# Optimization experiments

Hardware: AMD Instinct MI355X
Metric: run time of the kernel (lower is better)

## Reference

```python
import jax, jax.numpy as jnp
import numpy as np

N = 100000      # nodes
E = 1250000     # edges
D_IN = 64
D_OUT = 64


def _gconv(x, src, dst, W_rel, W_root, b, n_nodes):
    # PyG GraphConv (aggr='add'): out = lin_rel(sum_{j in N(i)} x_j) + lin_root(x_i)
    agg = jax.ops.segment_sum(x[src], dst, num_segments=n_nodes)  # [N, d]
    return agg @ W_rel + b + x @ W_root


def setup_inputs() -> dict:
    key = jax.random.key(0)
    ks = jax.random.split(key, 12)
    graph = jax.random.normal(ks[0], (N, D_IN), dtype=jnp.float32)
    edge_index = jax.random.randint(ks[1], (2, E), 0, N, dtype=jnp.int32)
    s_in = 1.0 / np.sqrt(D_IN)
    s_out = 1.0 / np.sqrt(D_OUT)
    d = {
        "graph": graph,
        "edge_index": edge_index,
        "W1_rel": jax.random.uniform(ks[2], (D_IN, D_OUT), jnp.float32, -s_in, s_in),
        "W1_root": jax.random.uniform(ks[3], (D_IN, D_OUT), jnp.float32, -s_in, s_in),
        "b1": jnp.zeros((D_OUT,), jnp.float32),
        "W2_rel": jax.random.uniform(ks[4], (D_OUT, D_OUT), jnp.float32, -s_out, s_out),
        "W2_root": jax.random.uniform(ks[5], (D_OUT, D_OUT), jnp.float32, -s_out, s_out),
        "b2": jnp.zeros((D_OUT,), jnp.float32),
        "W3_rel": jax.random.uniform(ks[6], (D_OUT, D_OUT), jnp.float32, -s_out, s_out),
        "W3_root": jax.random.uniform(ks[7], (D_OUT, D_OUT), jnp.float32, -s_out, s_out),
        "b3": jnp.zeros((D_OUT,), jnp.float32),
    }
    return d


def reference(graph, edge_index, W1_rel, W1_root, b1, W2_rel, W2_root, b2, W3_rel, W3_root, b3):
    src, dst = edge_index[0], edge_index[1]
    n = graph.shape[0]
    y1 = jax.nn.elu(_gconv(graph, src, dst, W1_rel, W1_root, b1, n))
    y2 = jax.nn.elu(_gconv(y1, src, dst, W2_rel, W2_root, b2, n))
    y3 = jax.nn.sigmoid(_gconv(y2, src, dst, W3_rel, W3_root, b3, n))
    return (y1, y2, y3)
```

## Files before the change

kernel.cpp:

```cpp
#include <hip/hip_runtime.h>
#include <hip/hip_bf16.h>
#include <math.h>


#define D 64
#define BSHIFT 9
#define BW 512
#define BCAP 8192

typedef __attribute__((ext_vector_type(8))) short short8;
typedef __attribute__((ext_vector_type(4))) float f32x4;

__device__ __forceinline__ ushort f2b(float f) {
    uint x = __float_as_uint(f);
    uint r = (x + 0x7fffu + ((x >> 16) & 1u)) >> 16;
    return (ushort)r;
}


__global__ __launch_bounds__(256) void convert_w(const float* __restrict__ w0,
                                                 const float* __restrict__ w1,
                                                 const float* __restrict__ w2,
                                                 const float* __restrict__ w3,
                                                 const float* __restrict__ w4,
                                                 const float* __restrict__ w5,
                                                 ushort* __restrict__ out,
                                                 int* __restrict__ bucketCnt,
                                                 ushort* __restrict__ hrel_zrow) {
    if (blockIdx.x == 0 && threadIdx.x < 256) bucketCnt[threadIdx.x] = 0;
    if (blockIdx.x == 1 && threadIdx.x < 32) ((uint*)hrel_zrow)[threadIdx.x] = 0;
    int m = blockIdx.x >> 4;
    int t = (blockIdx.x & 15) * 256 + threadIdx.x;
    const float* src = m == 0 ? w0 : m == 1 ? w1 : m == 2 ? w2 : m == 3 ? w3 : m == 4 ? w4 : w5;
    int k = t >> 6, d = t & 63;
    out[m * 4096 + d * 64 + k] = f2b(src[t]);
}


__global__ __launch_bounds__(1024) void bucket_scatter(const int* __restrict__ src,
                                                       const int* __restrict__ dst,
                                                       int* __restrict__ bucketCnt,
                                                       uint* __restrict__ store,
                                                       int E) {
    __shared__ int h[256], base[256], cur[256];
    int t = threadIdx.x;
    if (t < 256) { h[t] = 0; cur[t] = 0; }
    __syncthreads();
    int e = blockIdx.x * 1024 + t;
    uint rec = 0; int b = 0;
    bool ok = e < E;
    if (ok) {
        int s = src[e];
        int d = dst[e];
        b = d >> BSHIFT;
        rec = ((uint)(d & (BW - 1)) << 17) | (uint)s;
        atomicAdd(&h[b], 1);
    }
    __syncthreads();
    if (t < 256) base[t] = h[t] ? atomicAdd(&bucketCnt[t], h[t]) : 0;
    __syncthreads();
    if (ok) {
        int r = atomicAdd(&cur[b], 1);
        int pos = base[b] + r;
        if (pos < BCAP)
            store[(size_t)b * BCAP + pos] = rec;
    }
}


__global__ __launch_bounds__(256) void scan_buckets(const int* __restrict__ bucketCnt,
                                                    int* __restrict__ bucketBase,
                                                    int* __restrict__ offs,
                                                    int nb, int n, int E) {
    __shared__ int tmp[256];
    int t = threadIdx.x;
    int v = (t < nb) ? bucketCnt[t] : 0;
    tmp[t] = v;
    __syncthreads();
    for (int off = 1; off < 256; off <<= 1) {
        int add = (t >= off) ? tmp[t - off] : 0;
        __syncthreads();
        tmp[t] += add;
        __syncthreads();
    }
    if (t < nb) bucketBase[t] = tmp[t] - v;
    if (t == 0) offs[n] = E;
}


__global__ __launch_bounds__(1024) void bucket_build(const int* __restrict__ bucketCnt,
                                                     const int* __restrict__ bucketBase,
                                                     const uint* __restrict__ store,
                                                     int* __restrict__ offs,
                                                     int* __restrict__ src_sorted, int n) {
    __shared__ int h[BW], loc[BW], cur[BW];
    __shared__ uint se[BCAP];
    int b = blockIdx.x, t = threadIdx.x;
    int cnt = bucketCnt[b];
    if (cnt > BCAP) cnt = BCAP;
    int obase = bucketBase[b];
    int d0 = b << BSHIFT;
    int nd = n - d0;
    if (nd > BW) nd = BW;
    if (t < BW) { h[t] = 0; cur[t] = 0; }
    __syncthreads();
    for (int i = t; i < cnt; i += 1024) {
        uint p = store[(size_t)b * BCAP + i];
        se[i] = p;
        atomicAdd(&h[p >> 17], 1);
    }
    __syncthreads();
    if (t < BW) loc[t] = h[t];
    __syncthreads();
    for (int off = 1; off < BW; off <<= 1) {
        int add = (t < BW && t >= off) ? loc[t - off] : 0;
        __syncthreads();
        if (t < BW) loc[t] += add;
        __syncthreads();
    }
    if (t < nd) offs[d0 + t] = obase + loc[t] - h[t];
    __syncthreads();
    for (int i = t; i < cnt; i += 1024) {
        uint p = se[i];
        int dl = p >> 17;
        int r = atomicAdd(&cur[dl], 1);
        src_sorted[obase + loc[dl] - h[dl] + r] = (int)(p & 0x1FFFFu);
    }
}


__global__ __launch_bounds__(256) void gemm_ro(const float* __restrict__ x,
                                               const ushort* __restrict__ WtR,
                                               const ushort* __restrict__ WtO,
                                               const float* __restrict__ bias,
                                               ushort* __restrict__ hrel,
                                               ushort* __restrict__ hroot, int n) {
    __shared__ ushort hsR[4][16 * 64];
    __shared__ ushort hsO[4][16 * 64];
    int t = threadIdx.x;
    int w = t >> 6, l = t & 63;
    int i0 = blockIdx.x * 64 + w * 16;
    int lr = l & 15, kb = l >> 4;
    int row = i0 + lr;
    int rowc = row < n ? row : n - 1;

    short8 a[2];
#pragma unroll
    for (int s = 0; s < 2; ++s) {
        const float* p = x + (size_t)rowc * D + s * 32 + kb * 8;
        float4 u = *(const float4*)p;
        float4 v = *(const float4*)(p + 4);
        a[s][0] = f2b(u.x); a[s][1] = f2b(u.y); a[s][2] = f2b(u.z); a[s][3] = f2b(u.w);
        a[s][4] = f2b(v.x); a[s][5] = f2b(v.y); a[s][6] = f2b(v.z); a[s][7] = f2b(v.w);
    }

#pragma unroll
    for (int ct = 0; ct < 4; ++ct) {
        f32x4 accR = (f32x4){0.f, 0.f, 0.f, 0.f};
        f32x4 accO = (f32x4){0.f, 0.f, 0.f, 0.f};
#pragma unroll
        for (int s = 0; s < 2; ++s) {
            short8 bR = *(const short8*)(WtR + (ct * 16 + lr) * D + s * 32 + kb * 8);
            short8 bO = *(const short8*)(WtO + (ct * 16 + lr) * D + s * 32 + kb * 8);
            accR = __builtin_amdgcn_mfma_f32_16x16x32_bf16(a[s], bR, accR, 0, 0, 0);
            accO = __builtin_amdgcn_mfma_f32_16x16x32_bf16(a[s], bO, accO, 0, 0, 0);
        }
        float bv = bias[ct * 16 + lr];
#pragma unroll
        for (int i = 0; i < 4; ++i) {
            hsR[w][(kb * 4 + i) * 64 + ct * 16 + lr] = f2b(accR[i]);
            hsO[w][(kb * 4 + i) * 64 + ct * 16 + lr] = f2b(accO[i] + bv);
        }
    }
    __syncthreads();

    int r = l >> 2, ch = l & 3;
    int grow = i0 + r;
    if (grow < n) {
        const float4* spR = (const float4*)&hsR[w][r * 64 + ch * 16];
        const float4* spO = (const float4*)&hsO[w][r * 64 + ch * 16];
        float4 r0 = spR[0];
        float4 r1 = spR[1];
        float4 o0 = spO[0];
        float4 o1 = spO[1];
        *(float4*)(hrel + (size_t)grow * D + ch * 16) = r0;
        *(float4*)(hrel + (size_t)grow * D + ch * 16 + 8) = r1;
        *(float4*)(hroot + (size_t)grow * D + ch * 16) = o0;
        *(float4*)(hroot + (size_t)grow * D + ch * 16 + 8) = o1;
    }
}


template <int ACT>
__global__ __launch_bounds__(256) void agg_act(const ushort* __restrict__ hrel,
                                               const ushort* __restrict__ hroot,
                                               const int* __restrict__ offs,
                                               const int* __restrict__ srcs,
                                               float* __restrict__ y, int n) {
    int nA = blockIdx.x * 8 + (threadIdx.x >> 6) * 2;
    int l = threadIdx.x & 63;
    if (nA >= n) return;
    int nB = nA + 1;
    bool hasB = nB < n;
    int q = l >> 4, r = l & 15;

    int oA = offs[nA];
    int oB = offs[nA + 1];
    int oC = hasB ? offs[nA + 2] : oB;

    float a0 = 0.f, a1 = 0.f, a2 = 0.f, a3 = 0.f;
    float b0 = 0.f, b1 = 0.f, b2 = 0.f, b3 = 0.f;

    int eA = oA, eB = oB;
    while (eA < oB || eB < oC) {
#pragma unroll
        for (int k = 0; k < 4; ++k) {
            int ia = eA + k * 4 + q;
            int ib = eB + k * 4 + q;
            int sA = (ia < oB) ? srcs[ia] : n;
            int sB = (ib < oC) ? srcs[ib] : n;
            uint2 uA = *(const uint2*)(hrel + (size_t)sA * D + r * 4);
            uint2 uB = *(const uint2*)(hrel + (size_t)sB * D + r * 4);
            a0 += __uint_as_float(uA.x << 16);
            a1 += __uint_as_float(uA.x & 0xffff0000u);
            a2 += __uint_as_float(uA.y << 16);
            a3 += __uint_as_float(uA.y & 0xffff0000u);
            b0 += __uint_as_float(uB.x << 16);
            b1 += __uint_as_float(uB.x & 0xffff0000u);
            b2 += __uint_as_float(uB.y << 16);
            b3 += __uint_as_float(uB.y & 0xffff0000u);
        }
        eA += 16; eB += 16;
    }

    a0 += __shfl_xor(a0, 32); a0 += __shfl_xor(a0, 16);
    a1 += __shfl_xor(a1, 32); a1 += __shfl_xor(a1, 16);
    a2 += __shfl_xor(a2, 32); a2 += __shfl_xor(a2, 16);
    a3 += __shfl_xor(a3, 32); a3 += __shfl_xor(a3, 16);
    b0 += __shfl_xor(b0, 32); b0 += __shfl_xor(b0, 16);
    b1 += __shfl_xor(b1, 32); b1 += __shfl_xor(b1, 16);
    b2 += __shfl_xor(b2, 32); b2 += __shfl_xor(b2, 16);
    b3 += __shfl_xor(b3, 32); b3 += __shfl_xor(b3, 16);

    if (q < 2 && (q == 0 || hasB)) {
        int node = q == 0 ? nA : nB;
        float v0 = q == 0 ? a0 : b0;
        float v1 = q == 0 ? a1 : b1;
        float v2 = q == 0 ? a2 : b2;
        float v3 = q == 0 ? a3 : b3;
        uint2 hr = *(const uint2*)(hroot + (size_t)node * D + r * 4);
        v0 += __uint_as_float(hr.x << 16);
        v1 += __uint_as_float(hr.x & 0xffff0000u);
        v2 += __uint_as_float(hr.y << 16);
        v3 += __uint_as_float(hr.y & 0xffff0000u);
        if (ACT == 0) {
            v0 = v0 > 0.f ? v0 : __expf(v0) - 1.f;
            v1 = v1 > 0.f ? v1 : __expf(v1) - 1.f;
            v2 = v2 > 0.f ? v2 : __expf(v2) - 1.f;
            v3 = v3 > 0.f ? v3 : __expf(v3) - 1.f;
        } else {
            v0 = __builtin_amdgcn_rcpf(1.f + __expf(-v0));
            v1 = __builtin_amdgcn_rcpf(1.f + __expf(-v1));
            v2 = __builtin_amdgcn_rcpf(1.f + __expf(-v2));
            v3 = __builtin_amdgcn_rcpf(1.f + __expf(-v3));
        }
        float4 o; o.x = v0; o.y = v1; o.z = v2; o.w = v3;
        *(float4*)(y + (size_t)node * D + r * 4) = o;
    }
}


extern "C" void kernel_launch(void* const* d_in, const int* in_sizes, int n_in,
                              void* d_out, int out_size, void* d_ws, size_t ws_size,
                              hipStream_t stream) {
    const float* graph = (const float*)d_in[0];
    const int* eidx    = (const int*)d_in[1];
    const float* W1r = (const float*)d_in[2];
    const float* W1o = (const float*)d_in[3];
    const float* b1  = (const float*)d_in[4];
    const float* W2r = (const float*)d_in[5];
    const float* W2o = (const float*)d_in[6];
    const float* b2  = (const float*)d_in[7];
    const float* W3r = (const float*)d_in[8];
    const float* W3o = (const float*)d_in[9];
    const float* b3  = (const float*)d_in[10];

    int n = in_sizes[0] / D;
    int E = in_sizes[1] / 2;
    const int* src  = eidx;
    const int* dstl = eidx + E;
    int nb = (n + BW - 1) >> BSHIFT;

    char* w = (char*)d_ws;
    auto carve = [&](size_t bytes) {
        void* p = (void*)w;
        w += (bytes + 255) & ~(size_t)255;
        return p;
    };
    ushort* hrel  = (ushort*)carve((size_t)(n + 1) * D * sizeof(ushort));
    ushort* hroot = (ushort*)carve((size_t)n * D * sizeof(ushort));
    uint* store = (uint*)hrel;
    int* offs       = (int*)carve((size_t)(n + 1) * sizeof(int));
    int* src_sorted = (int*)carve((size_t)(E + 16) * sizeof(int));
    int* bucketCnt  = (int*)carve(256 * sizeof(int));
    int* bucketBase = (int*)carve(256 * sizeof(int));
    ushort* wt      = (ushort*)carve(6 * 4096 * sizeof(ushort));
    ushort* wtR1 = wt;
    ushort* wtO1 = wt + 1 * 4096;
    ushort* wtR2 = wt + 2 * 4096;
    ushort* wtO2 = wt + 3 * 4096;
    ushort* wtR3 = wt + 4 * 4096;
    ushort* wtO3 = wt + 5 * 4096;

    int eb1 = (E + 1023) / 1024;
    int tb  = (n + 63) / 64;
    int ab  = (n + 7) / 8;

    convert_w<<<96, 256, 0, stream>>>(W1r, W1o, W2r, W2o, W3r, W3o, wt, bucketCnt,
                                      hrel + (size_t)n * D);
    bucket_scatter<<<eb1, 1024, 0, stream>>>(src, dstl, bucketCnt, store, E);
    scan_buckets<<<1, 256, 0, stream>>>(bucketCnt, bucketBase, offs, nb, n, E);
    bucket_build<<<nb, 1024, 0, stream>>>(bucketCnt, bucketBase, store, offs, src_sorted, n);

    float* out = (float*)d_out;
    float* y1 = out;
    float* y2 = out + (size_t)n * D;
    float* y3 = out + 2 * (size_t)n * D;


    gemm_ro<<<tb, 256, 0, stream>>>(graph, wtR1, wtO1, b1, hrel, hroot, n);
    agg_act<0><<<ab, 256, 0, stream>>>(hrel, hroot, offs, src_sorted, y1, n);
    gemm_ro<<<tb, 256, 0, stream>>>(y1, wtR2, wtO2, b2, hrel, hroot, n);
    agg_act<0><<<ab, 256, 0, stream>>>(hrel, hroot, offs, src_sorted, y2, n);
    gemm_ro<<<tb, 256, 0, stream>>>(y2, wtR3, wtO3, b3, hrel, hroot, n);
    agg_act<1><<<ab, 256, 0, stream>>>(hrel, hroot, offs, src_sorted, y3, n);
}
```

Measured before the change: 316.5 us.

## Fuse edge bucket scatter with first-layer GEMM and fold bucket scan into build

Merges the edge bucket-scatter kernel and the first layer's dense transform into one launch, with block ranges split by role, so the two independent phases run concurrently. The bucket prefix scan now runs inside each bucket_build block, which drops a separate single-block kernel. The scatter staging buffer moves from hrel to the y3 output region so the first GEMM can write hrel at the same time. It also hoists the root-term load in the aggregation kernel ahead of the neighbour loop. In exchange, every build block repeats a small 256-entry scan, and the scatter now uses 256-thread blocks that each handle four edges per thread.

```diff
diff --git a/kernel.cpp b/kernel.cpp
--- a/kernel.cpp
+++ b/kernel.cpp
@@ -37,109 +37,16 @@
 }
 
 
-__global__ __launch_bounds__(1024) void bucket_scatter(const int* __restrict__ src,
-                                                       const int* __restrict__ dst,
-                                                       int* __restrict__ bucketCnt,
-                                                       uint* __restrict__ store,
-                                                       int E) {
-    __shared__ int h[256], base[256], cur[256];
-    int t = threadIdx.x;
-    if (t < 256) { h[t] = 0; cur[t] = 0; }
-    __syncthreads();
-    int e = blockIdx.x * 1024 + t;
-    uint rec = 0; int b = 0;
-    bool ok = e < E;
-    if (ok) {
-        int s = src[e];
-        int d = dst[e];
-        b = d >> BSHIFT;
-        rec = ((uint)(d & (BW - 1)) << 17) | (uint)s;
-        atomicAdd(&h[b], 1);
-    }
-    __syncthreads();
-    if (t < 256) base[t] = h[t] ? atomicAdd(&bucketCnt[t], h[t]) : 0;
-    __syncthreads();
-    if (ok) {
-        int r = atomicAdd(&cur[b], 1);
-        int pos = base[b] + r;
-        if (pos < BCAP)
-            store[(size_t)b * BCAP + pos] = rec;
-    }
-}
-
-
-__global__ __launch_bounds__(256) void scan_buckets(const int* __restrict__ bucketCnt,
-                                                    int* __restrict__ bucketBase,
-                                                    int* __restrict__ offs,
-                                                    int nb, int n, int E) {
-    __shared__ int tmp[256];
-    int t = threadIdx.x;
-    int v = (t < nb) ? bucketCnt[t] : 0;
-    tmp[t] = v;
-    __syncthreads();
-    for (int off = 1; off < 256; off <<= 1) {
-        int add = (t >= off) ? tmp[t - off] : 0;
-        __syncthreads();
-        tmp[t] += add;
-        __syncthreads();
-    }
-    if (t < nb) bucketBase[t] = tmp[t] - v;
-    if (t == 0) offs[n] = E;
-}
-
-
-__global__ __launch_bounds__(1024) void bucket_build(const int* __restrict__ bucketCnt,
-                                                     const int* __restrict__ bucketBase,
-                                                     const uint* __restrict__ store,
-                                                     int* __restrict__ offs,
-                                                     int* __restrict__ src_sorted, int n) {
-    __shared__ int h[BW], loc[BW], cur[BW];
-    __shared__ uint se[BCAP];
-    int b = blockIdx.x, t = threadIdx.x;
-    int cnt = bucketCnt[b];
-    if (cnt > BCAP) cnt = BCAP;
-    int obase = bucketBase[b];
-    int d0 = b << BSHIFT;
-    int nd = n - d0;
-    if (nd > BW) nd = BW;
-    if (t < BW) { h[t] = 0; cur[t] = 0; }
-    __syncthreads();
-    for (int i = t; i < cnt; i += 1024) {
-        uint p = store[(size_t)b * BCAP + i];
-        se[i] = p;
-        atomicAdd(&h[p >> 17], 1);
-    }
-    __syncthreads();
-    if (t < BW) loc[t] = h[t];
-    __syncthreads();
-    for (int off = 1; off < BW; off <<= 1) {
-        int add = (t < BW && t >= off) ? loc[t - off] : 0;
-        __syncthreads();
-        if (t < BW) loc[t] += add;
-        __syncthreads();
-    }
-    if (t < nd) offs[d0 + t] = obase + loc[t] - h[t];
-    __syncthreads();
-    for (int i = t; i < cnt; i += 1024) {
-        uint p = se[i];
-        int dl = p >> 17;
-        int r = atomicAdd(&cur[dl], 1);
-        src_sorted[obase + loc[dl] - h[dl] + r] = (int)(p & 0x1FFFFu);
-    }
-}
-
-
-__global__ __launch_bounds__(256) void gemm_ro(const float* __restrict__ x,
-                                               const ushort* __restrict__ WtR,
-                                               const ushort* __restrict__ WtO,
-                                               const float* __restrict__ bias,
-                                               ushort* __restrict__ hrel,
-                                               ushort* __restrict__ hroot, int n) {
-    __shared__ ushort hsR[4][16 * 64];
-    __shared__ ushort hsO[4][16 * 64];
-    int t = threadIdx.x;
+__device__ __forceinline__ void gemm_ro_body(int blk, int t,
+                                             const float* __restrict__ x,
+                                             const ushort* __restrict__ WtR,
+                                             const ushort* __restrict__ WtO,
+                                             const float* __restrict__ bias,
+                                             ushort* __restrict__ hrel,
+                                             ushort* __restrict__ hroot, int n,
+                                             ushort* hsR, ushort* hsO) {
     int w = t >> 6, l = t & 63;
-    int i0 = blockIdx.x * 64 + w * 16;
+    int i0 = blk * 64 + w * 16;
     int lr = l & 15, kb = l >> 4;
     int row = i0 + lr;
     int rowc = row < n ? row : n - 1;
@@ -154,6 +61,8 @@
         a[s][4] = f2b(v.x); a[s][5] = f2b(v.y); a[s][6] = f2b(v.z); a[s][7] = f2b(v.w);
     }
 
+    ushort* hR = hsR + w * 16 * 64;
+    ushort* hO = hsO + w * 16 * 64;
 #pragma unroll
     for (int ct = 0; ct < 4; ++ct) {
         f32x4 accR = (f32x4){0.f, 0.f, 0.f, 0.f};
@@ -168,8 +77,8 @@
         float bv = bias[ct * 16 + lr];
 #pragma unroll
         for (int i = 0; i < 4; ++i) {
-            hsR[w][(kb * 4 + i) * 64 + ct * 16 + lr] = f2b(accR[i]);
-            hsO[w][(kb * 4 + i) * 64 + ct * 16 + lr] = f2b(accO[i] + bv);
+            hR[(kb * 4 + i) * 64 + ct * 16 + lr] = f2b(accR[i]);
+            hO[(kb * 4 + i) * 64 + ct * 16 + lr] = f2b(accO[i] + bv);
         }
     }
     __syncthreads();
@@ -177,8 +86,8 @@
     int r = l >> 2, ch = l & 3;
     int grow = i0 + r;
     if (grow < n) {
-        const float4* spR = (const float4*)&hsR[w][r * 64 + ch * 16];
-        const float4* spO = (const float4*)&hsO[w][r * 64 + ch * 16];
+        const float4* spR = (const float4*)&hR[r * 64 + ch * 16];
+        const float4* spO = (const float4*)&hO[r * 64 + ch * 16];
         float4 r0 = spR[0];
         float4 r1 = spR[1];
         float4 o0 = spO[0];
@@ -187,6 +96,121 @@
         *(float4*)(hrel + (size_t)grow * D + ch * 16 + 8) = r1;
         *(float4*)(hroot + (size_t)grow * D + ch * 16) = o0;
         *(float4*)(hroot + (size_t)grow * D + ch * 16 + 8) = o1;
+    }
+}
+
+__global__ __launch_bounds__(256) void gemm_ro(const float* __restrict__ x,
+                                               const ushort* __restrict__ WtR,
+                                               const ushort* __restrict__ WtO,
+                                               const float* __restrict__ bias,
+                                               ushort* __restrict__ hrel,
+                                               ushort* __restrict__ hroot, int n) {
+    __shared__ ushort hsR[4 * 16 * 64];
+    __shared__ ushort hsO[4 * 16 * 64];
+    gemm_ro_body(blockIdx.x, threadIdx.x, x, WtR, WtO, bias, hrel, hroot, n, hsR, hsO);
+}
+
+
+__global__ __launch_bounds__(256) void scatter_gemm(const int* __restrict__ esrc,
+                                                    const int* __restrict__ edst,
+                                                    int* __restrict__ bucketCnt,
+                                                    uint* __restrict__ store,
+                                                    int E, int SB,
+                                                    const float* __restrict__ x,
+                                                    const ushort* __restrict__ WtR,
+                                                    const ushort* __restrict__ WtO,
+                                                    const float* __restrict__ bias,
+                                                    ushort* __restrict__ hrel,
+                                                    ushort* __restrict__ hroot, int n) {
+    __shared__ ushort hsR[4 * 16 * 64];
+    int t = threadIdx.x;
+    int bx = blockIdx.x;
+    if (bx >= SB) {
+        __shared__ ushort hsO[4 * 16 * 64];
+        gemm_ro_body(bx - SB, t, x, WtR, WtO, bias, hrel, hroot, n, hsR, hsO);
+        return;
+    }
+    int* h    = (int*)hsR;
+    int* base = h + 256;
+    int* cur  = base + 256;
+    if (t < 256) { h[t] = 0; cur[t] = 0; }
+    __syncthreads();
+    int e0 = bx * 1024;
+    uint rec[4]; int bb[4];
+#pragma unroll
+    for (int i = 0; i < 4; ++i) {
+        int e = e0 + i * 256 + t;
+        if (e < E) {
+            int s = esrc[e];
+            int d = edst[e];
+            bb[i] = d >> BSHIFT;
+            rec[i] = ((uint)(d & (BW - 1)) << 17) | (uint)s;
+            atomicAdd(&h[bb[i]], 1);
+        } else bb[i] = -1;
+    }
+    __syncthreads();
+    base[t] = h[t] ? atomicAdd(&bucketCnt[t], h[t]) : 0;
+    __syncthreads();
+#pragma unroll
+    for (int i = 0; i < 4; ++i) {
+        if (bb[i] >= 0) {
+            int p = base[bb[i]] + atomicAdd(&cur[bb[i]], 1);
+            if (p < BCAP)
+                store[(size_t)bb[i] * BCAP + p] = rec[i];
+        }
+    }
+}
+
+
+__global__ __launch_bounds__(1024) void bucket_build(const int* __restrict__ bucketCnt,
+                                                     const uint* __restrict__ store,
+                                                     int* __restrict__ offs,
+                                                     int* __restrict__ src_sorted,
+                                                     int n, int nb, int E) {
+    __shared__ int h[BW], loc[BW], cur[BW];
+    __shared__ int sc[256];
+    __shared__ uint se[BCAP];
+    int b = blockIdx.x, t = threadIdx.x;
+
+    if (t < 256) sc[t] = (t < nb) ? bucketCnt[t] : 0;
+    __syncthreads();
+    for (int off = 1; off < 256; off <<= 1) {
+        int add = (t < 256 && t >= off) ? sc[t - off] : 0;
+        __syncthreads();
+        if (t < 256) sc[t] += add;
+        __syncthreads();
+    }
+    int obase = sc[b] - bucketCnt[b];
+    if (b == 0 && t == 0) offs[n] = E;
+
+    int cnt = bucketCnt[b];
+    if (cnt > BCAP) cnt = BCAP;
+    int d0 = b << BSHIFT;
+    int nd = n - d0;
+    if (nd > BW) nd = BW;
+    if (t < BW) { h[t] = 0; cur[t] = 0; }
+    __syncthreads();
+    for (int i = t; i < cnt; i += 1024) {
+        uint p = store[(size_t)b * BCAP + i];
+        se[i] = p;
+        atomicAdd(&h[p >> 17], 1);
+    }
+    __syncthreads();
+    if (t < BW) loc[t] = h[t];
+    __syncthreads();
+    for (int off = 1; off < BW; off <<= 1) {
+        int add = (t < BW && t >= off) ? loc[t - off] : 0;
+        __syncthreads();
+        if (t < BW) loc[t] += add;
+        __syncthreads();
+    }
+    if (t < nd) offs[d0 + t] = obase + loc[t] - h[t];
+    __syncthreads();
+    for (int i = t; i < cnt; i += 1024) {
+        uint p = se[i];
+        int dl = p >> 17;
+        int r = atomicAdd(&cur[dl], 1);
+        src_sorted[obase + loc[dl] - h[dl] + r] = (int)(p & 0x1FFFFu);
     }
 }
 
@@ -207,6 +231,9 @@
     int oA = offs[nA];
     int oB = offs[nA + 1];
     int oC = hasB ? offs[nA + 2] : oB;
+
+    uint2 hrA = *(const uint2*)(hroot + (size_t)nA * D + r * 4);
+    uint2 hrB = hasB ? *(const uint2*)(hroot + (size_t)nB * D + r * 4) : hrA;
 
     float a0 = 0.f, a1 = 0.f, a2 = 0.f, a3 = 0.f;
     float b0 = 0.f, b1 = 0.f, b2 = 0.f, b3 = 0.f;
@@ -244,15 +271,11 @@
 
     if (q < 2 && (q == 0 || hasB)) {
         int node = q == 0 ? nA : nB;
-        float v0 = q == 0 ? a0 : b0;
-        float v1 = q == 0 ? a1 : b1;
-        float v2 = q == 0 ? a2 : b2;
-        float v3 = q == 0 ? a3 : b3;
-        uint2 hr = *(const uint2*)(hroot + (size_t)node * D + r * 4);
-        v0 += __uint_as_float(hr.x << 16);
-        v1 += __uint_as_float(hr.x & 0xffff0000u);
-        v2 += __uint_as_float(hr.y << 16);
-        v3 += __uint_as_float(hr.y & 0xffff0000u);
+        uint2 hr = q == 0 ? hrA : hrB;
+        float v0 = (q == 0 ? a0 : b0) + __uint_as_float(hr.x << 16);
+        float v1 = (q == 0 ? a1 : b1) + __uint_as_float(hr.x & 0xffff0000u);
+        float v2 = (q == 0 ? a2 : b2) + __uint_as_float(hr.y << 16);
+        float v3 = (q == 0 ? a3 : b3) + __uint_as_float(hr.y & 0xffff0000u);
         if (ACT == 0) {
             v0 = v0 > 0.f ? v0 : __expf(v0) - 1.f;
             v1 = v1 > 0.f ? v1 : __expf(v1) - 1.f;
@@ -287,8 +310,8 @@
 
     int n = in_sizes[0] / D;
     int E = in_sizes[1] / 2;
-    const int* src  = eidx;
-    const int* dstl = eidx + E;
+    const int* esrc = eidx;
+    const int* edst = eidx + E;
     int nb = (n + BW - 1) >> BSHIFT;
 
     char* w = (char*)d_ws;
@@ -299,11 +322,9 @@
     };
     ushort* hrel  = (ushort*)carve((size_t)(n + 1) * D * sizeof(ushort));
     ushort* hroot = (ushort*)carve((size_t)n * D * sizeof(ushort));
-    uint* store = (uint*)hrel;
     int* offs       = (int*)carve((size_t)(n + 1) * sizeof(int));
     int* src_sorted = (int*)carve((size_t)(E + 16) * sizeof(int));
     int* bucketCnt  = (int*)carve(256 * sizeof(int));
-    int* bucketBase = (int*)carve(256 * sizeof(int));
     ushort* wt      = (ushort*)carve(6 * 4096 * sizeof(ushort));
     ushort* wtR1 = wt;
     ushort* wtO1 = wt + 1 * 4096;
@@ -312,23 +333,22 @@
     ushort* wtR3 = wt + 4 * 4096;
     ushort* wtO3 = wt + 5 * 4096;
 
-    int eb1 = (E + 1023) / 1024;
-    int tb  = (n + 63) / 64;
-    int ab  = (n + 7) / 8;
-
-    convert_w<<<96, 256, 0, stream>>>(W1r, W1o, W2r, W2o, W3r, W3o, wt, bucketCnt,
-                                      hrel + (size_t)n * D);
-    bucket_scatter<<<eb1, 1024, 0, stream>>>(src, dstl, bucketCnt, store, E);
-    scan_buckets<<<1, 256, 0, stream>>>(bucketCnt, bucketBase, offs, nb, n, E);
-    bucket_build<<<nb, 1024, 0, stream>>>(bucketCnt, bucketBase, store, offs, src_sorted, n);
-
     float* out = (float*)d_out;
     float* y1 = out;
     float* y2 = out + (size_t)n * D;
     float* y3 = out + 2 * (size_t)n * D;
-
-
-    gemm_ro<<<tb, 256, 0, stream>>>(graph, wtR1, wtO1, b1, hrel, hroot, n);
+    uint* store = (uint*)y3;
+
+    int SB = (E + 1023) / 1024;
+    int tb = (n + 63) / 64;
+    int ab = (n + 7) / 8;
+
+    convert_w<<<96, 256, 0, stream>>>(W1r, W1o, W2r, W2o, W3r, W3o, wt, bucketCnt,
+                                      hrel + (size_t)n * D);
+    scatter_gemm<<<SB + tb, 256, 0, stream>>>(esrc, edst, bucketCnt, store, E, SB,
+                                              graph, wtR1, wtO1, b1, hrel, hroot, n);
+    bucket_build<<<nb, 1024, 0, stream>>>(bucketCnt, store, offs, src_sorted, n, nb, E);
+
     agg_act<0><<<ab, 256, 0, stream>>>(hrel, hroot, offs, src_sorted, y1, n);
     gemm_ro<<<tb, 256, 0, stream>>>(y1, wtR2, wtO2, b2, hrel, hroot, n);
     agg_act<0><<<ab, 256, 0, stream>>>(hrel, hroot, offs, src_sorted, y2, n);
```

New measurement: 313.7 us. Within noise of the previous version (-0.9%).
